# Performance work log

Measured on AMD Instinct MI355X. Metric: run time of the kernel, lower is better.

The kernel has to match this reference:

```python
import jax, jax.numpy as jnp
from jax import lax
import numpy as np

B, C, HH, WW = 8, 64, 128, 128
N = HH * WW
EPS = 1e-5


def _roll_h(xn, sign):
    # per-channel cyclic roll along H: out[b,c,h,w] = xn[b,c,(h - sign*c) % H, w]
    _, Cx, Hx, _ = xn.shape
    c = jnp.arange(Cx)[:, None]
    idx = (jnp.arange(Hx)[None, :] - sign * jnp.arange(Cx)[:, None]) % Hx  # (C,H)
    return xn[:, c, idx, :]


def _roll_w(xn, sign):
    return _roll_h(xn.transpose(0, 1, 3, 2), sign).transpose(0, 1, 3, 2)


def _ch_linear(xn, w, b):
    # nn.Linear over the channel dim of a BCHW tensor (token-MLP on (B,N,C))
    return jnp.einsum('bchw,cd->bdhw', xn, w) + b[None, :, None, None]


def _bn(xn, g, b):
    # BatchNorm2d, training-mode stats (biased var over B,H,W)
    m = xn.mean(axis=(0, 2, 3), keepdims=True)
    v = xn.var(axis=(0, 2, 3), keepdims=True)
    return (xn - m) * lax.rsqrt(v + EPS) * g[None, :, None, None] + b[None, :, None, None]


def _dwconv(xn, w, dil, pad):
    return lax.conv_general_dilated(xn, w, (1, 1), ((pad, pad), (pad, pad)),
                                    rhs_dilation=(dil, dil),
                                    dimension_numbers=('NCHW', 'OIHW', 'NCHW'),
                                    feature_group_count=xn.shape[1])


def _pc(xn, w):
    # 1x1 pointwise conv, no bias; w: (C_out, C_in)
    return jnp.einsum('bchw,oc->bohw', xn, w)


def lgff_forward(x, fc1_w, fc1_b, fc2_w, fc2_b, fc3_w, fc3_b, fc4_w, fc4_b,
                 fc5_w, fc5_b, ln_g, ln_b, pc_w, dw_w, dw_b, dw_bn_g, dw_bn_b,
                 dd_w, dd_bn_g, dd_bn_b, se_w1, se_b1, se_w2, se_b2, H, W):
    Bx, Nx, Cx = x.shape
    xn = x.transpose(0, 2, 1).reshape(Bx, Cx, H, W)
    # branch 1: roll+c along H -> fc1 -> GELU -> roll+c along W -> fc2
    a = jax.nn.gelu(_ch_linear(_roll_h(xn, 1), fc1_w, fc1_b), approximate=False)
    x_1 = _ch_linear(_roll_w(a, 1), fc2_w, fc2_b) + xn
    # branch 2: roll-c along W -> fc3 -> GELU -> roll+c along H -> fc4
    b = jax.nn.gelu(_ch_linear(_roll_w(xn, -1), fc3_w, fc3_b), approximate=False)
    x_2 = _ch_linear(_roll_h(b, 1), fc4_w, fc4_b) + xn
    # concat along feature dim (token layout dim=2 == channel dim here), LayerNorm(2C), fc5
    xc = jnp.concatenate([x_1, x_2], axis=1)  # (B, 2C, H, W)
    m = xc.mean(axis=1, keepdims=True)
    v = xc.var(axis=1, keepdims=True)
    xc = (xc - m) * lax.rsqrt(v + EPS) * ln_g[None, :, None, None] + ln_b[None, :, None, None]
    x1 = _ch_linear(xc, fc5_w, fc5_b) + xn
    # conv fusion part
    x2 = _pc(x1, pc_w)
    y = jax.nn.relu(_bn(_dwconv(x2, dw_w, 1, 1) + dw_b[None, :, None, None], dw_bn_g, dw_bn_b))
    y = jax.nn.relu(_bn(_dwconv(y, dd_w, 2, 2), dd_bn_g, dd_bn_b))
    y = _pc(y, pc_w)
    # four branches x3..x6 share identical weights/input -> identical outputs
    x7 = 4.0 * (x2 * y)
    # SE block
    s = x7.mean(axis=(2, 3), keepdims=True)  # (B,C,1,1)
    e = jax.nn.relu(jnp.einsum('bcij,oc->boij', s, se_w1) + se_b1[None, :, None, None])
    e = jax.nn.sigmoid(jnp.einsum('bcij,oc->boij', e, se_w2) + se_b2[None, :, None, None])
    return x7 + x7 * e  # (B, C, H, W)


def setup_inputs():
    key = jax.random.key(0)
    ks = jax.random.split(key, 12)
    r = C // 8
    inp = {
        'x': jax.random.normal(ks[0], (B, N, C), jnp.float32),
        'fc1_w': jax.random.normal(ks[1], (C, C), jnp.float32) * 0.02,
        'fc1_b': jnp.zeros((C,), jnp.float32),
        'fc2_w': jax.random.normal(ks[2], (C, C), jnp.float32) * 0.02,
        'fc2_b': jnp.zeros((C,), jnp.float32),
        'fc3_w': jax.random.normal(ks[3], (C, C), jnp.float32) * 0.02,
        'fc3_b': jnp.zeros((C,), jnp.float32),
        'fc4_w': jax.random.normal(ks[4], (C, C), jnp.float32) * 0.02,
        'fc4_b': jnp.zeros((C,), jnp.float32),
        'fc5_w': jax.random.normal(ks[5], (2 * C, C), jnp.float32) * 0.02,
        'fc5_b': jnp.zeros((C,), jnp.float32),
        'ln_g': jnp.ones((2 * C,), jnp.float32),
        'ln_b': jnp.zeros((2 * C,), jnp.float32),
        'pc_w': jax.random.normal(ks[6], (C, C), jnp.float32) * np.sqrt(2.0 / C).astype(np.float32),
        'dw_w': jax.random.normal(ks[7], (C, 1, 3, 3), jnp.float32) * np.sqrt(2.0 / 9.0).astype(np.float32),
        'dw_b': jnp.zeros((C,), jnp.float32),
        'dw_bn_g': jnp.ones((C,), jnp.float32),
        'dw_bn_b': jnp.zeros((C,), jnp.float32),
        'dd_w': jax.random.normal(ks[8], (C, 1, 3, 3), jnp.float32) * np.sqrt(2.0 / 9.0).astype(np.float32),
        'dd_bn_g': jnp.ones((C,), jnp.float32),
        'dd_bn_b': jnp.zeros((C,), jnp.float32),
        'se_w1': jax.random.normal(ks[9], (r, C), jnp.float32) * np.sqrt(2.0 / r).astype(np.float32),
        'se_b1': jnp.zeros((r,), jnp.float32),
        'se_w2': jax.random.normal(ks[10], (C, r), jnp.float32) * np.sqrt(2.0 / C).astype(np.float32),
        'se_b2': jnp.zeros((C,), jnp.float32),
        'H': HH,
        'W': WW,
    }
    return inp


def reference(x, fc1_w, fc1_b, fc2_w, fc2_b, fc3_w, fc3_b, fc4_w, fc4_b,
              fc5_w, fc5_b, ln_g, ln_b, pc_w, dw_w, dw_b, dw_bn_g, dw_bn_b,
              dd_w, dd_bn_g, dd_bn_b, se_w1, se_b1, se_w2, se_b2, H, W):
    return lgff_forward(x, fc1_w, fc1_b, fc2_w, fc2_b, fc3_w, fc3_b, fc4_w, fc4_b,
                        fc5_w, fc5_b, ln_g, ln_b, pc_w, dw_w, dw_b, dw_bn_g, dw_bn_b,
                        dd_w, dd_bn_g, dd_bn_b, se_w1, se_b1, se_w2, se_b2, H, W)
```

## Files before the change

kernel.cpp:

```cpp
#include <hip/hip_runtime.h>

constexpr int NB  = 8;
constexpr int NC  = 64;
constexpr int NH  = 128;
constexpr int NW  = 128;
constexpr int NHW = NH * NW;
constexpr int CHW = NC * NHW;
constexpr int SZ  = NB * CHW;
constexpr int NPOS = NB * NHW;
constexpr float EPS = 1e-5f;

typedef unsigned short u16;
using bf8   = __attribute__((ext_vector_type(8))) short;
using u16x8 = __attribute__((ext_vector_type(8))) u16;
using u16x4 = __attribute__((ext_vector_type(4))) u16;
using f32x4 = __attribute__((ext_vector_type(4))) float;

static __device__ inline short f2bf(float f) {
    union { float f; unsigned int u; } v; v.f = f;
    unsigned int r = v.u + 0x7fffu + ((v.u >> 16) & 1u);
    return (short)(r >> 16);
}
static __device__ inline float bf2f(u16 u) {
    union { unsigned int i; float f; } v; v.i = ((unsigned int)u) << 16;
    return v.f;
}

__global__ void k_transpose(const float* __restrict__ x, u16* __restrict__ xn) {
    __shared__ float t[64 * 65];
    int b   = blockIdx.x >> 8;
    int hw0 = (blockIdx.x & 255) << 6;
    int tid = threadIdx.x;
    #pragma unroll
    for (int k = 0; k < 16; ++k) {
        int idx = tid + (k << 8);
        int c = idx & 63, hwl = idx >> 6;
        t[c * 65 + hwl] = x[((size_t)b * NHW + hw0 + hwl) * NC + c];
    }
    __syncthreads();
    #pragma unroll
    for (int k = 0; k < 16; ++k) {
        int idx = tid + (k << 8);
        int hwl = idx & 63, c = idx >> 6;
        xn[(size_t)(b * NC + c) * NHW + hw0 + hwl] = (u16)f2bf(t[c * 65 + hwl]);
    }
}

__global__ void k_pq(const float* __restrict__ w5, const float* __restrict__ lng,
                     const float* __restrict__ lnb, float* __restrict__ PQ) {
    int d = threadIdx.x;
    float P = 0.f, Q = 0.f;
    for (int c = 0; c < 128; ++c) {
        float wv = w5[c * 64 + d];
        P += lng[c] * wv;
        Q += lnb[c] * wv;
    }
    PQ[d] = P; PQ[64 + d] = Q;
}

__global__ __launch_bounds__(512) void
k_mfc2(const u16* __restrict__ xn,
       const float* __restrict__ w1, const float* __restrict__ b1,
       const float* __restrict__ w3, const float* __restrict__ b3,
       u16* __restrict__ t1, u16* __restrict__ t2) {
    __shared__ short wA[64 * 64];
    __shared__ short wB[64 * 64];
    int tid = threadIdx.x;
    int l = tid & 63, wv = tid >> 6;
    int q = l >> 4, col = l & 15;

    {
        const float* wsrc = (wv < 4) ? w1 : w3;
        short* wdst = (wv < 4) ? wA : wB;
        int wv4 = wv & 3;
        #pragma unroll
        for (int i = 0; i < 8; ++i) {
            int c0 = wv4 * 2 + i * 8;
            unsigned int pk = (unsigned int)(u16)f2bf(wsrc[c0 * 64 + l]) |
                              ((unsigned int)(u16)f2bf(wsrc[(c0 + 1) * 64 + l]) << 16);
            *(unsigned int*)&wdst[l * 64 + (c0 ^ ((l & 7) << 3))] = pk;
        }
    }
    __syncthreads();

    int p  = blockIdx.x * 128 + wv * 16 + col;
    int b  = p >> 14;
    int hw = p & (NHW - 1);
    int h  = hw >> 7, w = hw & 127;
    const u16* inb = xn + (size_t)b * CHW;

    f32x4 acc1[4], acc2[4];
    #pragma unroll
    for (int dt = 0; dt < 4; ++dt) {
        acc1[dt] = (f32x4){0.f, 0.f, 0.f, 0.f};
        acc2[dt] = (f32x4){0.f, 0.f, 0.f, 0.f};
    }
    #pragma unroll
    for (int ks = 0; ks < 2; ++ks) {
        bf8 f1, f2;
        #pragma unroll
        for (int j = 0; j < 8; ++j) {
            int c = ks * 32 + q * 8 + j;
            f1[j] = (short)inb[c * NHW + (((h - c) & 127) << 7) + w];
            f2[j] = (short)inb[c * NHW + (h << 7) + ((w + c) & 127)];
        }
        #pragma unroll
        for (int dt = 0; dt < 4; ++dt) {
            int d = dt * 16 + col;
            int wo = (ks * 32 + q * 8) ^ ((d & 7) << 3);
            acc1[dt] = __builtin_amdgcn_mfma_f32_16x16x32_bf16(f1, *(bf8*)&wA[d * 64 + wo], acc1[dt], 0, 0, 0);
            acc2[dt] = __builtin_amdgcn_mfma_f32_16x16x32_bf16(f2, *(bf8*)&wB[d * 64 + wo], acc2[dt], 0, 0, 0);
        }
    }

    int hwst = (blockIdx.x * 128 + wv * 16 + q * 4) & (NHW - 1);
    size_t ob = (size_t)b * CHW + hwst;
    #pragma unroll
    for (int dt = 0; dt < 4; ++dt) {
        int d = dt * 16 + col;
        float bb1 = b1[d], bb3 = b3[d];
        u16x4 o1v, o2v;
        #pragma unroll
        for (int r = 0; r < 4; ++r) {
            float v1 = acc1[dt][r] + bb1;
            v1 = 0.5f * v1 * (1.f + erff(v1 * 0.70710678118654752f));
            float v2 = acc2[dt][r] + bb3;
            v2 = 0.5f * v2 * (1.f + erff(v2 * 0.70710678118654752f));
            o1v[r] = (u16)f2bf(v1);
            o2v[r] = (u16)f2bf(v2);
        }
        *(u16x4*)&t1[ob + (size_t)d * NHW] = o1v;
        *(u16x4*)&t2[ob + (size_t)d * NHW] = o2v;
    }
}

__global__ __launch_bounds__(512) void
k_ffuse(const u16* __restrict__ t1, const u16* __restrict__ t2,
        const u16* __restrict__ xnb,
        const float* __restrict__ fc2w, const float* __restrict__ fc2b,
        const float* __restrict__ fc4w, const float* __restrict__ fc4b,
        const float* __restrict__ w5, const float* __restrict__ lng,
        const float* __restrict__ PQ, const float* __restrict__ b5,
        u16* __restrict__ x1out) {
    __shared__ short wA[64 * 64];
    __shared__ short wB[64 * 64];
    __shared__ short wG[64 * 128];
    __shared__ short xt[128 * 140];

    int tid = threadIdx.x;
    int l = tid & 63, wv = tid >> 6;
    int q = l >> 4, col = l & 15;

    {
        const float* wsrc = (wv < 4) ? fc2w : fc4w;
        short* wdst = (wv < 4) ? wA : wB;
        int wv4 = wv & 3;
        #pragma unroll
        for (int i = 0; i < 8; ++i) {
            int c0 = wv4 * 2 + i * 8;
            unsigned int pk = (unsigned int)(u16)f2bf(wsrc[c0 * 64 + l]) |
                              ((unsigned int)(u16)f2bf(wsrc[(c0 + 1) * 64 + l]) << 16);
            *(unsigned int*)&wdst[l * 64 + (c0 ^ ((l & 7) << 3))] = pk;
        }
    }
    #pragma unroll
    for (int i = 0; i < 8; ++i) {
        int c0 = wv * 2 + i * 16;
        unsigned int pk = (unsigned int)(u16)f2bf(lng[c0] * w5[c0 * 64 + l]) |
                          ((unsigned int)(u16)f2bf(lng[c0 + 1] * w5[(c0 + 1) * 64 + l]) << 16);
        *(unsigned int*)&wG[l * 128 + (c0 ^ ((l & 7) << 3))] = pk;
    }
    __syncthreads();

    int p  = blockIdx.x * 128 + wv * 16 + col;
    int b  = p >> 14;
    int hw = p & (NHW - 1);
    int h  = hw >> 7, w = hw & 127;
    size_t base = (size_t)b * CHW;
    int pos = wv * 16 + col;

    f32x4 acc1[4], acc2[4];
    #pragma unroll
    for (int dt = 0; dt < 4; ++dt) {
        acc1[dt] = (f32x4){0.f, 0.f, 0.f, 0.f};
        acc2[dt] = (f32x4){0.f, 0.f, 0.f, 0.f};
    }
    #pragma unroll
    for (int ks = 0; ks < 2; ++ks) {
        bf8 f1, f2;
        #pragma unroll
        for (int j = 0; j < 8; ++j) {
            int c = ks * 32 + q * 8 + j;
            f1[j] = (short)t1[base + c * NHW + (h << 7) + ((w - c) & 127)];
            f2[j] = (short)t2[base + c * NHW + (((h - c) & 127) << 7) + w];
        }
        #pragma unroll
        for (int dt = 0; dt < 4; ++dt) {
            int d = dt * 16 + col;
            int wo = (ks * 32 + q * 8) ^ ((d & 7) << 3);
            acc1[dt] = __builtin_amdgcn_mfma_f32_16x16x32_bf16(*(bf8*)&wA[d * 64 + wo], f1, acc1[dt], 0, 0, 0);
            acc2[dt] = __builtin_amdgcn_mfma_f32_16x16x32_bf16(*(bf8*)&wB[d * 64 + wo], f2, acc2[dt], 0, 0, 0);
        }
    }

    float xr[16];
    #pragma unroll
    for (int dt = 0; dt < 4; ++dt)
        #pragma unroll
        for (int r = 0; r < 4; ++r)
            xr[dt * 4 + r] = bf2f(xnb[base + (size_t)(dt * 16 + q * 4 + r) * NHW + hw]);

    float s = 0.f, sq = 0.f;
    #pragma unroll
    for (int dt = 0; dt < 4; ++dt) {
        float v1[4], v2[4];
        #pragma unroll
        for (int r = 0; r < 4; ++r) {
            int d = dt * 16 + q * 4 + r;
            v1[r] = acc1[dt][r] + fc2b[d] + xr[dt * 4 + r];
            v2[r] = acc2[dt][r] + fc4b[d] + xr[dt * 4 + r];
            s += v1[r] + v2[r];
            sq += v1[r] * v1[r] + v2[r] * v2[r];
        }
        unsigned int pk0 = (unsigned int)(u16)f2bf(v1[0]) | ((unsigned int)(u16)f2bf(v1[1]) << 16);
        unsigned int pk1 = (unsigned int)(u16)f2bf(v1[2]) | ((unsigned int)(u16)f2bf(v1[3]) << 16);
        *(uint2*)&xt[pos * 140 + dt * 16 + q * 4] = make_uint2(pk0, pk1);
        unsigned int pk2 = (unsigned int)(u16)f2bf(v2[0]) | ((unsigned int)(u16)f2bf(v2[1]) << 16);
        unsigned int pk3 = (unsigned int)(u16)f2bf(v2[2]) | ((unsigned int)(u16)f2bf(v2[3]) << 16);
        *(uint2*)&xt[pos * 140 + 64 + dt * 16 + q * 4] = make_uint2(pk2, pk3);
    }
    s  += __shfl_xor(s, 16);  s += __shfl_xor(s, 32);
    sq += __shfl_xor(sq, 16); sq += __shfl_xor(sq, 32);
    float m    = s * (1.f / 128.f);
    float var  = sq * (1.f / 128.f) - m * m;
    float rstd = rsqrtf(var + EPS);
    float mr   = m * rstd;
    __syncthreads();

    f32x4 acc[4];
    #pragma unroll
    for (int dt = 0; dt < 4; ++dt) acc[dt] = (f32x4){0.f, 0.f, 0.f, 0.f};
    #pragma unroll
    for (int ks = 0; ks < 4; ++ks) {
        bf8 bfr = *(bf8*)&xt[pos * 140 + ks * 32 + q * 8];
        #pragma unroll
        for (int dt = 0; dt < 4; ++dt) {
            int d = dt * 16 + col;
            bf8 afr = *(bf8*)&wG[d * 128 + ((ks * 32 + q * 8) ^ ((d & 7) << 3))];
            acc[dt] = __builtin_amdgcn_mfma_f32_16x16x32_bf16(afr, bfr, acc[dt], 0, 0, 0);
        }
    }

    size_t obase = base + hw;
    #pragma unroll
    for (int dt = 0; dt < 4; ++dt) {
        #pragma unroll
        for (int r = 0; r < 4; ++r) {
            int d = dt * 16 + q * 4 + r;
            float val = rstd * acc[dt][r] + PQ[64 + d] - mr * PQ[d] + b5[d] + xr[dt * 4 + r];
            x1out[obase + (size_t)d * NHW] = (u16)f2bf(val);
        }
    }
}

template<bool BNRELU_IN>
__global__ __launch_bounds__(512) void
k_mfc(const u16* __restrict__ in, const float* __restrict__ wgt,
      const float* __restrict__ psum, const float* __restrict__ psq,
      const float* __restrict__ bng, const float* __restrict__ bnb,
      u16* __restrict__ out) {
    __shared__ short wt[64 * 64];
    __shared__ float scl[64], sft[64];
    int tid = threadIdx.x;
    int l = tid & 63, wv = tid >> 6;
    int q = l >> 4, col = l & 15;

    #pragma unroll
    for (int i = 0; i < 8; ++i) {
        int d = wv * 8 + i;
        wt[d * 64 + (l ^ ((d & 7) << 3))] = f2bf(wgt[d * 64 + l]);
    }
    if (BNRELU_IN && tid < 64) {
        float s = 0.f, qv = 0.f;
        #pragma unroll
        for (int i = 0; i < 32; ++i) {
            int bb = i >> 2, j = i & 3;
            int idx = ((bb * 64 + tid) << 2) + j;
            s += psum[idx]; qv += psq[idx];
        }
        const float inv = 1.f / (float)(NB * NHW);
        float m = s * inv;
        float var = qv * inv - m * m;
        float rs = rsqrtf(var + EPS);
        float sc = rs * bng[tid];
        scl[tid] = sc;
        sft[tid] = bnb[tid] - m * sc;
    }
    __syncthreads();

    int p  = blockIdx.x * 128 + wv * 16 + col;
    int b  = p >> 14;
    int hw = p & (NHW - 1);
    const u16* inb = in + (size_t)b * CHW;

    f32x4 acc[4];
    #pragma unroll
    for (int dt = 0; dt < 4; ++dt) acc[dt] = (f32x4){0.f, 0.f, 0.f, 0.f};

    #pragma unroll
    for (int ks = 0; ks < 2; ++ks) {
        bf8 bfr;
        #pragma unroll
        for (int j = 0; j < 8; ++j) {
            int c = ks * 32 + q * 8 + j;
            u16 raw = inb[c * NHW + hw];
            if (BNRELU_IN) {
                float v = fmaxf(bf2f(raw) * scl[c] + sft[c], 0.f);
                bfr[j] = f2bf(v);
            } else {
                bfr[j] = (short)raw;
            }
        }
        #pragma unroll
        for (int dt = 0; dt < 4; ++dt) {
            int d = dt * 16 + col;
            bf8 afr = *(bf8*)&wt[d * 64 + ((ks * 32 + q * 8) ^ ((d & 7) << 3))];
            acc[dt] = __builtin_amdgcn_mfma_f32_16x16x32_bf16(bfr, afr, acc[dt], 0, 0, 0);
        }
    }

    int hwst = (blockIdx.x * 128 + wv * 16 + q * 4) & (NHW - 1);
    size_t ob = (size_t)b * CHW + hwst;
    #pragma unroll
    for (int dt = 0; dt < 4; ++dt) {
        int d = dt * 16 + col;
        u16x4 ov;
        #pragma unroll
        for (int r = 0; r < 4; ++r) ov[r] = (u16)f2bf(acc[dt][r]);
        *(u16x4*)&out[ob + (size_t)d * NHW] = ov;
    }
}

template<int DIL, bool HASBIAS, bool BNIN>
__global__ __launch_bounds__(256) void
k_dwlds(const u16* __restrict__ in, const float* __restrict__ wgt,
        const float* __restrict__ bias,
        const float* __restrict__ psumIn, const float* __restrict__ psqIn,
        const float* __restrict__ bng, const float* __restrict__ bnb,
        u16* __restrict__ out, float* __restrict__ psumOut, float* __restrict__ psqOut) {
    constexpr int STR = 136;
    __shared__ float tile[36 * STR];
    __shared__ float ss[256], sq[256];

    int blk = ((blockIdx.x & 7) << 8) | (blockIdx.x >> 3);
    int q   = blk & 3;
    int bc  = blk >> 2;
    int c   = bc & 63;
    int r0  = q * 32;
    int tid = threadIdx.x;
    const u16* ip = in + (size_t)bc * NHW;

    float scale = 0.f, shift = 0.f;
    if (BNIN) {
        float s = 0.f, qv = 0.f;
        #pragma unroll
        for (int i = 0; i < 32; ++i) {
            int bb = i >> 2, j = i & 3;
            int idx = ((bb * 64 + c) << 2) + j;
            s += psumIn[idx]; qv += psqIn[idx];
        }
        const float inv = 1.f / (float)(NB * NHW);
        float m = s * inv;
        float var = qv * inv - m * m;
        float rs = rsqrtf(var + EPS);
        scale = rs * bng[c];
        shift = bnb[c] - m * scale;
    }

    #pragma unroll 1
    for (int idx = tid; idx < 36 * 16; idx += 256) {
        int lr = idx >> 4, u = idx & 15;
        int gr = r0 - 2 + lr;
        float v[8] = {0.f, 0.f, 0.f, 0.f, 0.f, 0.f, 0.f, 0.f};
        if (gr >= 0 && gr < NH) {
            u16x8 raw = *(const u16x8*)(ip + gr * NW + u * 8);
            #pragma unroll
            for (int j = 0; j < 8; ++j) {
                float f = bf2f(raw[j]);
                if (BNIN) f = fmaxf(f * scale + shift, 0.f);
                v[j] = f;
            }
        }
        *(float4*)&tile[lr * STR + 4 + u * 8]     = make_float4(v[0], v[1], v[2], v[3]);
        *(float4*)&tile[lr * STR + 4 + u * 8 + 4] = make_float4(v[4], v[5], v[6], v[7]);
        if (u == 0)  *(float4*)&tile[lr * STR]       = make_float4(0.f, 0.f, 0.f, 0.f);
        if (u == 15) *(float4*)&tile[lr * STR + 132] = make_float4(0.f, 0.f, 0.f, 0.f);
    }
    __syncthreads();

    float wc[9];
    #pragma unroll
    for (int k = 0; k < 9; ++k) wc[k] = wgt[c * 9 + k];

    int row  = tid >> 3;
    int col0 = (tid & 7) * 16;
    float o[16];
    float bb = HASBIAS ? bias[c] : 0.f;
    #pragma unroll
    for (int j = 0; j < 16; ++j) o[j] = bb;

    #pragma unroll
    for (int i = 0; i < 3; ++i) {
        const float* rp = &tile[(row + 2 + (i - 1) * DIL) * STR + 4 + col0];
        float4 A  = *(const float4*)(rp - 4);
        float4 B0 = *(const float4*)(rp);
        float4 B1 = *(const float4*)(rp + 4);
        float4 B2 = *(const float4*)(rp + 8);
        float4 B3 = *(const float4*)(rp + 12);
        float4 Cc = *(const float4*)(rp + 16);
        float ww[24] = {A.x,A.y,A.z,A.w, B0.x,B0.y,B0.z,B0.w, B1.x,B1.y,B1.z,B1.w,
                        B2.x,B2.y,B2.z,B2.w, B3.x,B3.y,B3.z,B3.w, Cc.x,Cc.y,Cc.z,Cc.w};
        float w0 = wc[3 * i], w1 = wc[3 * i + 1], w2 = wc[3 * i + 2];
        #pragma unroll
        for (int j = 0; j < 16; ++j)
            o[j] += w0 * ww[4 + j - DIL] + w1 * ww[4 + j] + w2 * ww[4 + j + DIL];
    }

    u16* op = out + (size_t)bc * NHW + (r0 + row) * NW + col0;
    u16x8 o1, o2;
    #pragma unroll
    for (int j = 0; j < 8; ++j) { o1[j] = (u16)f2bf(o[j]); o2[j] = (u16)f2bf(o[8 + j]); }
    *(u16x8*)(op)     = o1;
    *(u16x8*)(op + 8) = o2;

    float s = 0.f, qq = 0.f;
    #pragma unroll
    for (int j = 0; j < 16; ++j) { s += o[j]; qq += o[j] * o[j]; }
    ss[tid] = s; sq[tid] = qq; __syncthreads();
    for (int off = 128; off > 0; off >>= 1) {
        if (tid < off) { ss[tid] += ss[tid + off]; sq[tid] += sq[tid + off]; }
        __syncthreads();
    }
    if (tid == 0) { psumOut[blk] = ss[0]; psqOut[blk] = sq[0]; }
}

__global__ void k_se_reduce(const u16* __restrict__ x2, const u16* __restrict__ y3,
                            float* __restrict__ s4) {
    __shared__ float ss[256];
    int q   = blockIdx.x & 3;
    int bc  = blockIdx.x >> 2;
    int tid = threadIdx.x;
    const u16* a  = x2 + (size_t)bc * NHW + q * (NHW / 4);
    const u16* b_ = y3 + (size_t)bc * NHW + q * (NHW / 4);
    float acc = 0.f;
    #pragma unroll
    for (int i = 0; i < 2; ++i) {
        u16x8 av = *(const u16x8*)(a + (tid + i * 256) * 8);
        u16x8 bv = *(const u16x8*)(b_ + (tid + i * 256) * 8);
        #pragma unroll
        for (int j = 0; j < 8; ++j) acc += bf2f(av[j]) * bf2f(bv[j]);
    }
    ss[tid] = acc; __syncthreads();
    for (int o = 128; o > 0; o >>= 1) {
        if (tid < o) ss[tid] += ss[tid + o];
        __syncthreads();
    }
    if (tid == 0) s4[blockIdx.x] = ss[0];
}

__global__ void k_final8(const u16* __restrict__ x2, const u16* __restrict__ y3,
                         const float* __restrict__ s4,
                         const float* __restrict__ w1, const float* __restrict__ b1,
                         const float* __restrict__ w2, const float* __restrict__ b2,
                         float* __restrict__ out) {
    __shared__ float sh[64], e1[8], ev[1];
    int tid = threadIdx.x;
    int bc = blockIdx.x >> 3;
    int b  = bc >> 6, c = bc & 63;

    if (tid < 64) {
        float sv = 0.f;
        #pragma unroll
        for (int j = 0; j < 4; ++j) sv += s4[(b * 64 + tid) * 4 + j];
        sh[tid] = sv * (4.f / (float)NHW);
    }
    __syncthreads();
    if (tid < 8) {
        float a = b1[tid];
        for (int cc = 0; cc < 64; ++cc) a += sh[cc] * w1[tid * 64 + cc];
        e1[tid] = a > 0.f ? a : 0.f;
    }
    __syncthreads();
    if (tid == 0) {
        float a = b2[c];
        #pragma unroll
        for (int j = 0; j < 8; ++j) a += e1[j] * w2[c * 8 + j];
        ev[0] = 1.f / (1.f + expf(-a));
    }
    __syncthreads();

    int t = blockIdx.x * 256 + tid;
    float f = 4.f * (1.f + ev[0]);
    u16x8 av = *(const u16x8*)(x2 + (size_t)t * 8);
    u16x8 bv = *(const u16x8*)(y3 + (size_t)t * 8);
    float4 o0, o1;
    o0.x = f * bf2f(av[0]) * bf2f(bv[0]); o0.y = f * bf2f(av[1]) * bf2f(bv[1]);
    o0.z = f * bf2f(av[2]) * bf2f(bv[2]); o0.w = f * bf2f(av[3]) * bf2f(bv[3]);
    o1.x = f * bf2f(av[4]) * bf2f(bv[4]); o1.y = f * bf2f(av[5]) * bf2f(bv[5]);
    o1.z = f * bf2f(av[6]) * bf2f(bv[6]); o1.w = f * bf2f(av[7]) * bf2f(bv[7]);
    *(float4*)(out + (size_t)t * 8)     = o0;
    *(float4*)(out + (size_t)t * 8 + 4) = o1;
}

extern "C" void kernel_launch(void* const* d_in, const int* in_sizes, int n_in,
                              void* d_out, int out_size, void* d_ws, size_t ws_size,
                              hipStream_t stream) {
    const float* x     = (const float*)d_in[0];
    const float* fc1w  = (const float*)d_in[1];
    const float* fc1b  = (const float*)d_in[2];
    const float* fc2w  = (const float*)d_in[3];
    const float* fc2b  = (const float*)d_in[4];
    const float* fc3w  = (const float*)d_in[5];
    const float* fc3b  = (const float*)d_in[6];
    const float* fc4w  = (const float*)d_in[7];
    const float* fc4b  = (const float*)d_in[8];
    const float* fc5w  = (const float*)d_in[9];
    const float* fc5b  = (const float*)d_in[10];
    const float* lng   = (const float*)d_in[11];
    const float* lnb   = (const float*)d_in[12];
    const float* pcw   = (const float*)d_in[13];
    const float* dww   = (const float*)d_in[14];
    const float* dwb   = (const float*)d_in[15];
    const float* dwbng = (const float*)d_in[16];
    const float* dwbnb = (const float*)d_in[17];
    const float* ddw   = (const float*)d_in[18];
    const float* ddbng = (const float*)d_in[19];
    const float* ddbnb = (const float*)d_in[20];
    const float* sew1  = (const float*)d_in[21];
    const float* seb1  = (const float*)d_in[22];
    const float* sew2  = (const float*)d_in[23];
    const float* seb2  = (const float*)d_in[24];

    float* out = (float*)d_out;
    u16* wsu = (u16*)d_ws;
    u16* bufA = wsu;
    u16* bufB = wsu + (size_t)SZ;
    u16* bufC = wsu + (size_t)2 * SZ;
    u16* bufD = wsu + (size_t)3 * SZ;
    float* st = (float*)(wsu + (size_t)4 * SZ);
    float* psumA = st;
    float* psqA  = st + 2048;
    float* psumB = st + 4096;
    float* psqB  = st + 6144;
    float* svec  = st + 8192;
    float* pqv   = st + 10240;

    dim3 blk(256);
    dim3 blk512(512);
    const float* nil = nullptr;

    k_transpose<<<NB * (NHW / 64), blk, 0, stream>>>(x, bufA);
    k_pq<<<1, 64, 0, stream>>>(fc5w, lng, lnb, pqv);
    k_mfc2<<<NPOS / 128, blk512, 0, stream>>>(bufA, fc1w, fc1b, fc3w, fc3b, bufB, bufC);
    k_ffuse<<<NPOS / 128, blk512, 0, stream>>>(bufB, bufC, bufA, fc2w, fc2b, fc4w, fc4b,
                                               fc5w, lng, pqv, fc5b, bufD);
    k_mfc<false><<<NPOS / 128, blk512, 0, stream>>>(bufD, pcw, nil, nil, nil, nil, bufA);
    k_dwlds<1, true, false><<<2048, blk, 0, stream>>>(bufA, dww, dwb, nil, nil, nil, nil, bufB, psumA, psqA);
    k_dwlds<2, false, true><<<2048, blk, 0, stream>>>(bufB, ddw, nil, psumA, psqA, dwbng, dwbnb, bufC, psumB, psqB);
    k_mfc<true><<<NPOS / 128, blk512, 0, stream>>>(bufC, pcw, psumB, psqB, ddbng, ddbnb, bufD);
    k_se_reduce<<<NB * NC * 4, blk, 0, stream>>>(bufA, bufD, svec);
    k_final8<<<SZ / 2048, blk, 0, stream>>>(bufA, bufD, svec, sew1, seb1, sew2, seb2, out);
}
```

Before: 141.2 us.

## Fuse SE dot-product reduction into final pointwise conv and swizzle block order

The separate SE reduction kernel, which re-read two full bf16 tensors, is removed. The second pointwise-conv kernel now computes per-block partial channel sums of x2*y3 directly from its output tile and writes them to a partial buffer, and a tiny kernel finishes the per-batch reduction. Block indices in the MFMA kernels are also remapped so consecutive blocks land in different batches, which changes the scheduling and cache locality pattern. The change saves a full read pass over two tensors and one launch, at the cost of an extra x2 load and a block-wide reduction inside the conv kernel.

```diff
diff --git a/kernel.cpp b/kernel.cpp
--- a/kernel.cpp
+++ b/kernel.cpp
@@ -68,6 +68,7 @@
     int tid = threadIdx.x;
     int l = tid & 63, wv = tid >> 6;
     int q = l >> 4, col = l & 15;
+    int bid = ((blockIdx.x & 7) << 7) | (blockIdx.x >> 3);
 
     {
         const float* wsrc = (wv < 4) ? w1 : w3;
@@ -83,7 +84,7 @@
     }
     __syncthreads();
 
-    int p  = blockIdx.x * 128 + wv * 16 + col;
+    int p  = bid * 128 + wv * 16 + col;
     int b  = p >> 14;
     int hw = p & (NHW - 1);
     int h  = hw >> 7, w = hw & 127;
@@ -113,7 +114,7 @@
         }
     }
 
-    int hwst = (blockIdx.x * 128 + wv * 16 + q * 4) & (NHW - 1);
+    int hwst = (bid * 128 + wv * 16 + q * 4) & (NHW - 1);
     size_t ob = (size_t)b * CHW + hwst;
     #pragma unroll
     for (int dt = 0; dt < 4; ++dt) {
@@ -150,6 +151,7 @@
     int tid = threadIdx.x;
     int l = tid & 63, wv = tid >> 6;
     int q = l >> 4, col = l & 15;
+    int bid = ((blockIdx.x & 7) << 7) | (blockIdx.x >> 3);
 
     {
         const float* wsrc = (wv < 4) ? fc2w : fc4w;
@@ -172,7 +174,7 @@
     }
     __syncthreads();
 
-    int p  = blockIdx.x * 128 + wv * 16 + col;
+    int p  = bid * 128 + wv * 16 + col;
     int b  = p >> 14;
     int hw = p & (NHW - 1);
     int h  = hw >> 7, w = hw & 127;
@@ -263,17 +265,20 @@
     }
 }
 
-template<bool BNRELU_IN>
+template<bool BNRELU_IN, bool SEPART>
 __global__ __launch_bounds__(512) void
 k_mfc(const u16* __restrict__ in, const float* __restrict__ wgt,
       const float* __restrict__ psum, const float* __restrict__ psq,
       const float* __restrict__ bng, const float* __restrict__ bnb,
+      const u16* __restrict__ x2in, float* __restrict__ gpart,
       u16* __restrict__ out) {
     __shared__ short wt[64 * 64];
     __shared__ float scl[64], sft[64];
+    __shared__ float spart[8][64];
     int tid = threadIdx.x;
     int l = tid & 63, wv = tid >> 6;
     int q = l >> 4, col = l & 15;
+    int bid = ((blockIdx.x & 7) << 7) | (blockIdx.x >> 3);
 
     #pragma unroll
     for (int i = 0; i < 8; ++i) {
@@ -298,7 +303,7 @@
     }
     __syncthreads();
 
-    int p  = blockIdx.x * 128 + wv * 16 + col;
+    int p  = bid * 128 + wv * 16 + col;
     int b  = p >> 14;
     int hw = p & (NHW - 1);
     const u16* inb = in + (size_t)b * CHW;
@@ -329,8 +334,9 @@
         }
     }
 
-    int hwst = (blockIdx.x * 128 + wv * 16 + q * 4) & (NHW - 1);
+    int hwst = (bid * 128 + wv * 16 + q * 4) & (NHW - 1);
     size_t ob = (size_t)b * CHW + hwst;
+    float pp[4] = {0.f, 0.f, 0.f, 0.f};
     #pragma unroll
     for (int dt = 0; dt < 4; ++dt) {
         int d = dt * 16 + col;
@@ -338,7 +344,38 @@
         #pragma unroll
         for (int r = 0; r < 4; ++r) ov[r] = (u16)f2bf(acc[dt][r]);
         *(u16x4*)&out[ob + (size_t)d * NHW] = ov;
-    }
+        if (SEPART) {
+            u16x4 xv = *(const u16x4*)&x2in[ob + (size_t)d * NHW];
+            #pragma unroll
+            for (int r = 0; r < 4; ++r) pp[dt] += bf2f(xv[r]) * bf2f(ov[r]);
+        }
+    }
+
+    if (SEPART) {
+        #pragma unroll
+        for (int dt = 0; dt < 4; ++dt) {
+            pp[dt] += __shfl_xor(pp[dt], 16);
+            pp[dt] += __shfl_xor(pp[dt], 32);
+        }
+        if (l < 16) {
+            #pragma unroll
+            for (int dt = 0; dt < 4; ++dt) spart[wv][dt * 16 + l] = pp[dt];
+        }
+        __syncthreads();
+        if (tid < 64) {
+            float s = 0.f;
+            #pragma unroll
+            for (int w8 = 0; w8 < 8; ++w8) s += spart[w8][tid];
+            gpart[(size_t)bid * 64 + tid] = s;
+        }
+    }
+}
+
+__global__ void k_se_fin(const float* __restrict__ gpart, float* __restrict__ svec) {
+    int b = blockIdx.x, c = threadIdx.x;
+    float s = 0.f;
+    for (int k = 0; k < 128; ++k) s += gpart[(size_t)(b * 128 + k) * 64 + c];
+    svec[b * 64 + c] = s * (4.f / (float)NHW);
 }
 
 template<int DIL, bool HASBIAS, bool BNIN>
@@ -444,32 +481,8 @@
     if (tid == 0) { psumOut[blk] = ss[0]; psqOut[blk] = sq[0]; }
 }
 
-__global__ void k_se_reduce(const u16* __restrict__ x2, const u16* __restrict__ y3,
-                            float* __restrict__ s4) {
-    __shared__ float ss[256];
-    int q   = blockIdx.x & 3;
-    int bc  = blockIdx.x >> 2;
-    int tid = threadIdx.x;
-    const u16* a  = x2 + (size_t)bc * NHW + q * (NHW / 4);
-    const u16* b_ = y3 + (size_t)bc * NHW + q * (NHW / 4);
-    float acc = 0.f;
-    #pragma unroll
-    for (int i = 0; i < 2; ++i) {
-        u16x8 av = *(const u16x8*)(a + (tid + i * 256) * 8);
-        u16x8 bv = *(const u16x8*)(b_ + (tid + i * 256) * 8);
-        #pragma unroll
-        for (int j = 0; j < 8; ++j) acc += bf2f(av[j]) * bf2f(bv[j]);
-    }
-    ss[tid] = acc; __syncthreads();
-    for (int o = 128; o > 0; o >>= 1) {
-        if (tid < o) ss[tid] += ss[tid + o];
-        __syncthreads();
-    }
-    if (tid == 0) s4[blockIdx.x] = ss[0];
-}
-
 __global__ void k_final8(const u16* __restrict__ x2, const u16* __restrict__ y3,
-                         const float* __restrict__ s4,
+                         const float* __restrict__ svec,
                          const float* __restrict__ w1, const float* __restrict__ b1,
                          const float* __restrict__ w2, const float* __restrict__ b2,
                          float* __restrict__ out) {
@@ -478,12 +491,7 @@
     int bc = blockIdx.x >> 3;
     int b  = bc >> 6, c = bc & 63;
 
-    if (tid < 64) {
-        float sv = 0.f;
-        #pragma unroll
-        for (int j = 0; j < 4; ++j) sv += s4[(b * 64 + tid) * 4 + j];
-        sh[tid] = sv * (4.f / (float)NHW);
-    }
+    if (tid < 64) sh[tid] = svec[b * 64 + tid];
     __syncthreads();
     if (tid < 8) {
         float a = b1[tid];
@@ -553,21 +561,24 @@
     float* psumB = st + 4096;
     float* psqB  = st + 6144;
     float* svec  = st + 8192;
-    float* pqv   = st + 10240;
+    float* pqv   = st + 8704;
+    float* gpart = st + 8832;
 
     dim3 blk(256);
     dim3 blk512(512);
     const float* nil = nullptr;
+    const u16*   nilu = nullptr;
+    float*       nilf = nullptr;
 
     k_transpose<<<NB * (NHW / 64), blk, 0, stream>>>(x, bufA);
     k_pq<<<1, 64, 0, stream>>>(fc5w, lng, lnb, pqv);
     k_mfc2<<<NPOS / 128, blk512, 0, stream>>>(bufA, fc1w, fc1b, fc3w, fc3b, bufB, bufC);
     k_ffuse<<<NPOS / 128, blk512, 0, stream>>>(bufB, bufC, bufA, fc2w, fc2b, fc4w, fc4b,
                                                fc5w, lng, pqv, fc5b, bufD);
-    k_mfc<false><<<NPOS / 128, blk512, 0, stream>>>(bufD, pcw, nil, nil, nil, nil, bufA);
+    k_mfc<false, false><<<NPOS / 128, blk512, 0, stream>>>(bufD, pcw, nil, nil, nil, nil, nilu, nilf, bufA);
     k_dwlds<1, true, false><<<2048, blk, 0, stream>>>(bufA, dww, dwb, nil, nil, nil, nil, bufB, psumA, psqA);
     k_dwlds<2, false, true><<<2048, blk, 0, stream>>>(bufB, ddw, nil, psumA, psqA, dwbng, dwbnb, bufC, psumB, psqB);
-    k_mfc<true><<<NPOS / 128, blk512, 0, stream>>>(bufC, pcw, psumB, psqB, ddbng, ddbnb, bufD);
-    k_se_reduce<<<NB * NC * 4, blk, 0, stream>>>(bufA, bufD, svec);
+    k_mfc<true, true><<<NPOS / 128, blk512, 0, stream>>>(bufC, pcw, psumB, psqB, ddbng, ddbnb, bufA, gpart, bufD);
+    k_se_fin<<<NB, 64, 0, stream>>>(gpart, svec);
     k_final8<<<SZ / 2048, blk, 0, stream>>>(bufA, bufD, svec, sew1, seb1, sew2, seb2, out);
 }
```

After: 140.7 us. Within noise of the previous version (-0.4%).
